# Kernel optimization log

Measured on AMD Instinct MI355X. Metric: run time of the kernel, lower is better.

Reference implementation:

```python
import jax, jax.numpy as jnp
from jax import lax
import numpy as np

B, CIN, COUT, N, H, W = 16, 64, 64, 8, 128, 128


def setup_inputs() -> dict:
    key = jax.random.key(0)
    ks = jax.random.split(key, 6)
    s = 0.05
    return {
        "x": jax.random.normal(ks[0], (B, CIN, H, W), dtype=jnp.float32),
        "condition": jax.random.normal(ks[1], (B, CIN), dtype=jnp.float32),
        "filt_w": jax.random.normal(ks[2], (N, COUT, CIN, 3, 3), dtype=jnp.float32) * s,
        "filt_b": jax.random.normal(ks[3], (N, COUT), dtype=jnp.float32) * s,
        "sel_w": jax.random.normal(ks[4], (N, CIN), dtype=jnp.float32) * s,
        "sel_b": jax.random.normal(ks[5], (N,), dtype=jnp.float32) * s,
    }


def reference(x, condition, filt_w, filt_b, sel_w, sel_b):
    b = x.shape[0]
    # condition selector: Linear(in_channels -> num_conditions) + softmax
    logits = condition.reshape(b, -1) @ sel_w.T + sel_b          # [B, N]
    weights = jax.nn.softmax(logits, axis=-1)                    # [B, N]

    n, cout, cin, kh, kw = filt_w.shape
    # Run all N branch convs in ONE conv by stacking filters on the output-channel axis.
    kern = filt_w.reshape(n * cout, cin, kh, kw)
    y = lax.conv_general_dilated(
        x, kern, window_strides=(1, 1), padding="SAME",
        dimension_numbers=("NCHW", "OIHW", "NCHW"))              # [B, N*COUT, H, W]
    h, w = y.shape[-2], y.shape[-1]
    y = y.reshape(b, n, cout, h, w) + filt_b.reshape(1, n, cout, 1, 1)
    # softmax-gated sum over the N branches
    out = jnp.einsum("bn,bnohw->bohw", weights, y)
    return out
```

## Files before the change

kernel.cpp:

```cpp
#include <hip/hip_runtime.h>
#include <stdint.h>

#define BATCH 16
#define CIN   64
#define COUT  64
#define NBR   8
#define HH    128
#define WW    128
#define XBH   130
#define XBW   130

typedef __attribute__((ext_vector_type(8)))  short short8;
typedef __attribute__((ext_vector_type(16))) float f32x16;

__device__ __forceinline__ unsigned int f2bf_hi(float f) {
    union { float f; uint32_t u; } v; v.f = f;
    return (v.u + 0x8000u) >> 16;
}
__device__ __forceinline__ unsigned short f2bf(float f) {
    union { float f; uint32_t u; } v; v.f = f;
    uint32_t u = v.u;
    return (unsigned short)((u + 0x7FFFu + ((u >> 16) & 1u)) >> 16);
}
__device__ __forceinline__ short8 gld_frag(const unsigned short* p) {
    union { uint4 u; short8 s; } t;
    t.u = *(const uint4*)p;
    return t.s;
}
__device__ __forceinline__ short8 lds_frag(const unsigned short* p) {
    union { uint2 u[2]; short8 s; } t;
    t.u[0] = *(const uint2*)p;
    t.u[1] = *(const uint2*)(p + 4);
    return t.s;
}

__global__ __launch_bounds__(256)
void k_prep(const float* __restrict__ cond,
            const float* __restrict__ sel_w,
            const float* __restrict__ sel_b,
            const float* __restrict__ filt_w,
            const float* __restrict__ filt_b,
            unsigned short* __restrict__ wfilt,
            float* __restrict__ cbias) {
    __shared__ float4 lw4[NBR * 144];
    __shared__ float lg[NBR];
    float* lw = (float*)lw4;

    const int blk = blockIdx.x;
    const int b = blk >> 6, o = blk & 63;
    const int tid = threadIdx.x;

    const float4* src4 = (const float4*)filt_w;
    #pragma unroll
    for (int i = tid; i < NBR * 144; i += 256)
        lw4[i] = src4[((i / 144) * COUT + o) * 144 + (i % 144)];

    {
        const int lane = tid & 63, w = tid >> 6;
        const float c0 = cond[b * CIN + lane];
        #pragma unroll
        for (int k = 0; k < 2; ++k) {
            const int n = w + k * 4;
            float p = c0 * sel_w[n * CIN + lane];
            #pragma unroll
            for (int off = 32; off > 0; off >>= 1)
                p += __shfl_down(p, off, 64);
            if (lane == 0) lg[n] = p + sel_b[n];
        }
    }
    __syncthreads();

    float w8[NBR];
    {
        float m = -1e30f;
        #pragma unroll
        for (int n = 0; n < NBR; ++n) m = fmaxf(m, lg[n]);
        float s = 0.f;
        #pragma unroll
        for (int n = 0; n < NBR; ++n) { w8[n] = __expf(lg[n] - m); s += w8[n]; }
        const float inv = 1.f / s;
        #pragma unroll
        for (int n = 0; n < NBR; ++n) w8[n] *= inv;
    }

    #pragma unroll
    for (int idx = tid; idx < 576; idx += 256) {
        const int t = idx >> 6, c = idx & 63;
        float acc = 0.f;
        #pragma unroll
        for (int n = 0; n < NBR; ++n)
            acc += w8[n] * lw[n * 576 + c * 9 + t];
        wfilt[(((long)(b * 9 + t) * COUT + o) << 6) + c] = f2bf(acc);
    }
    if (tid == 0) {
        float ab = 0.f;
        #pragma unroll
        for (int n = 0; n < NBR; ++n) ab += w8[n] * filt_b[n * COUT + o];
        cbias[b * COUT + o] = ab;
    }
}

__global__ __launch_bounds__(256)
void k_cast(const float* __restrict__ x, unsigned short* __restrict__ xb) {
    const int b   = blockIdx.y;
    const int hp  = blockIdx.x;
    const int tid = threadIdx.x;
    unsigned short* dst = xb + ((long)(b * XBH + hp) * XBW) * 64;
    const bool zrow = (hp == 0) || (hp == XBH - 1);
    const int h = hp - 1;
    const long cs = (long)HH * WW;

    for (int t = tid; t < XBW * 8; t += 256) {
        const int wp = t >> 3, q = t & 7;
        uint4 v; v.x = v.y = v.z = v.w = 0u;
        if (!zrow && wp != 0 && wp != XBW - 1) {
            const float* px = x + (((long)(b * CIN + q * 8)) * HH + h) * WW + (wp - 1);
            v.x = f2bf_hi(px[0])      | (f2bf_hi(px[cs])     << 16);
            v.y = f2bf_hi(px[2 * cs]) | (f2bf_hi(px[3 * cs]) << 16);
            v.z = f2bf_hi(px[4 * cs]) | (f2bf_hi(px[5 * cs]) << 16);
            v.w = f2bf_hi(px[6 * cs]) | (f2bf_hi(px[7 * cs]) << 16);
        }
        *(uint4*)&dst[t * 8] = v;
    }
}

#define RT 8
#define WT 32
#define SLABW 34
#define SLABR 10
#define PSTR  68

__global__ __launch_bounds__(256, 2)
void k_conv4(const unsigned short* __restrict__ xb,
             const unsigned short* __restrict__ wfilt,
             const float* __restrict__ cbias,
             float* __restrict__ out) {
    __shared__ unsigned short lx[SLABR * SLABW * PSTR];

    const int b  = blockIdx.z;
    const int h0 = blockIdx.y * RT;
    const int w0 = blockIdx.x * WT;
    const int tid = threadIdx.x;

    const unsigned short* xbb = xb + (long)b * XBH * XBW * 64;
    for (int t = tid; t < SLABR * SLABW * 8; t += 256) {
        const int s = t / (SLABW * 8);
        const int i = t - s * (SLABW * 8);
        const int p = i >> 3;
        const int q = i & 7;
        const uint4 v = *(const uint4*)(xbb + (((h0 + s) * XBW + w0 + p) << 6) + (q << 3));
        uint2 u0, u1;
        u0.x = v.x; u0.y = v.y; u1.x = v.z; u1.y = v.w;
        unsigned short* lp = &lx[(s * SLABW + p) * PSTR + (q << 3)];
        *(uint2*)lp       = u0;
        *(uint2*)(lp + 4) = u1;
    }

    const int lane = tid & 63;
    const int wave = tid >> 6;
    const int l31  = lane & 31;
    const int lh   = lane >> 5;
    const int r0   = wave * 2;

    const unsigned short* wf = wfilt + (long)b * 9 * COUT * CIN;

    short8 A0[4], A1[4];
    #pragma unroll
    for (int cc = 0; cc < 4; ++cc) {
        A0[cc] = gld_frag(wf + l31 * CIN + cc * 16 + lh * 8);
        A1[cc] = gld_frag(wf + (32 + l31) * CIN + cc * 16 + lh * 8);
    }

    f32x16 acc00, acc01, acc10, acc11;
    #pragma unroll
    for (int i = 0; i < 16; ++i) {
        const int m = (i & 3) + 8 * (i >> 2) + 4 * lh;
        const float b0 = cbias[b * COUT + m];
        const float b1 = cbias[b * COUT + 32 + m];
        acc00[i] = b0; acc01[i] = b0;
        acc10[i] = b1; acc11[i] = b1;
    }

    __syncthreads();

    #pragma unroll
    for (int tap = 0; tap < 9; ++tap) {
        short8 nA0[4], nA1[4];
        if (tap < 8) {
            const unsigned short* wn = wf + (long)(tap + 1) * COUT * CIN;
            #pragma unroll
            for (int cc = 0; cc < 4; ++cc) {
                nA0[cc] = gld_frag(wn + l31 * CIN + cc * 16 + lh * 8);
                nA1[cc] = gld_frag(wn + (32 + l31) * CIN + cc * 16 + lh * 8);
            }
        }
        const int kh = tap / 3, kw = tap % 3;
        #pragma unroll
        for (int cc = 0; cc < 4; ++cc) {
            const int kofs = cc * 16 + lh * 8;
            short8 b0 = lds_frag(&lx[((r0     + kh) * SLABW + l31 + kw) * PSTR + kofs]);
            short8 b1 = lds_frag(&lx[((r0 + 1 + kh) * SLABW + l31 + kw) * PSTR + kofs]);
            acc00 = __builtin_amdgcn_mfma_f32_32x32x16_bf16(A0[cc], b0, acc00, 0, 0, 0);
            acc01 = __builtin_amdgcn_mfma_f32_32x32x16_bf16(A0[cc], b1, acc01, 0, 0, 0);
            acc10 = __builtin_amdgcn_mfma_f32_32x32x16_bf16(A1[cc], b0, acc10, 0, 0, 0);
            acc11 = __builtin_amdgcn_mfma_f32_32x32x16_bf16(A1[cc], b1, acc11, 0, 0, 0);
        }
        #pragma unroll
        for (int cc = 0; cc < 4; ++cc) { A0[cc] = nA0[cc]; A1[cc] = nA1[cc]; }
    }

    #pragma unroll
    for (int cb = 0; cb < 2; ++cb) {
        #pragma unroll
        for (int pb = 0; pb < 2; ++pb) {
            const f32x16 v = cb == 0 ? (pb == 0 ? acc00 : acc01)
                                     : (pb == 0 ? acc10 : acc11);
            const int hrow = h0 + r0 + pb;
            float* op = out + (((long)(b * COUT + cb * 32) * HH + hrow) * WW + w0 + l31);
            #pragma unroll
            for (int i = 0; i < 16; ++i) {
                const int m = (i & 3) + 8 * (i >> 2) + 4 * lh;
                op[(long)m * HH * WW] = v[i];
            }
        }
    }
}

extern "C" void kernel_launch(void* const* d_in, const int* in_sizes, int n_in,
                              void* d_out, int out_size, void* d_ws, size_t ws_size,
                              hipStream_t stream) {
    const float* x      = (const float*)d_in[0];
    const float* cond   = (const float*)d_in[1];
    const float* filt_w = (const float*)d_in[2];
    const float* filt_b = (const float*)d_in[3];
    const float* sel_w  = (const float*)d_in[4];
    const float* sel_b  = (const float*)d_in[5];
    float* out = (float*)d_out;

    float*          cbias = (float*)d_ws;
    unsigned short* wfilt = (unsigned short*)((char*)d_ws + 4096);
    unsigned short* xb    = (unsigned short*)((char*)d_ws + 4096 + 1179648);

    k_prep<<<BATCH * COUT, 256, 0, stream>>>(cond, sel_w, sel_b, filt_w, filt_b, wfilt, cbias);

    dim3 cg(XBH, BATCH);
    k_cast<<<cg, 256, 0, stream>>>(x, xb);

    dim3 grid(WW / WT, HH / RT, BATCH);
    k_conv4<<<grid, 256, 0, stream>>>(xb, wfilt, cbias, out);
}
```

Measured before the change: 184.1 us.

## Pre-tile input slabs with swizzle, load via global_load_lds, merge prep kernels

The prep and cast kernels are merged into one launch. The cast half now writes the bf16 input pre-arranged as per-tile halo slabs with an XOR swizzle on the channel groups. The conv kernel copies each slab straight into LDS using global_load_lds 16-byte transfers and reads B fragments as single 128-bit LDS loads, with the swizzle intended to avoid bank conflicts. Occupancy hint rises to 3 blocks per SM because the unpadded LDS footprint is smaller. In exchange, the halo duplication makes the intermediate buffer larger and the cast does more global writes.

```diff
diff --git a/kernel.cpp b/kernel.cpp
--- a/kernel.cpp
+++ b/kernel.cpp
@@ -7,8 +7,14 @@
 #define NBR   8
 #define HH    128
 #define WW    128
-#define XBH   130
-#define XBW   130
+
+#define RT 8
+#define WT 32
+#define SLABW 34
+#define SLABR 10
+#define SLABPIX (SLABR * SLABW)
+#define SLABUS  (SLABPIX * 64)
+#define NTILES  (BATCH * (HH / RT) * (WW / WT))
 
 typedef __attribute__((ext_vector_type(8)))  short short8;
 typedef __attribute__((ext_vector_type(16))) float f32x16;
@@ -27,133 +33,133 @@
     t.u = *(const uint4*)p;
     return t.s;
 }
-__device__ __forceinline__ short8 lds_frag(const unsigned short* p) {
-    union { uint2 u[2]; short8 s; } t;
-    t.u[0] = *(const uint2*)p;
-    t.u[1] = *(const uint2*)(p + 4);
+__device__ __forceinline__ short8 lds_frag128(const unsigned short* p) {
+    union { uint4 u; short8 s; } t;
+    t.u = *(const uint4*)p;
     return t.s;
 }
+__device__ __forceinline__ void gload_lds16(const unsigned short* g, unsigned short* l) {
+    __builtin_amdgcn_global_load_lds(
+        (const __attribute__((address_space(1))) unsigned int*)g,
+        (__attribute__((address_space(3))) unsigned int*)l, 16, 0, 0);
+}
 
 __global__ __launch_bounds__(256)
-void k_prep(const float* __restrict__ cond,
-            const float* __restrict__ sel_w,
-            const float* __restrict__ sel_b,
-            const float* __restrict__ filt_w,
-            const float* __restrict__ filt_b,
-            unsigned short* __restrict__ wfilt,
-            float* __restrict__ cbias) {
+void k_pc(const float* __restrict__ cond,
+          const float* __restrict__ sel_w,
+          const float* __restrict__ sel_b,
+          const float* __restrict__ filt_w,
+          const float* __restrict__ filt_b,
+          const float* __restrict__ x,
+          unsigned short* __restrict__ wfilt,
+          float* __restrict__ cbias,
+          unsigned short* __restrict__ xt) {
     __shared__ float4 lw4[NBR * 144];
     __shared__ float lg[NBR];
-    float* lw = (float*)lw4;
-
-    const int blk = blockIdx.x;
-    const int b = blk >> 6, o = blk & 63;
     const int tid = threadIdx.x;
 
-    const float4* src4 = (const float4*)filt_w;
-    #pragma unroll
-    for (int i = tid; i < NBR * 144; i += 256)
-        lw4[i] = src4[((i / 144) * COUT + o) * 144 + (i % 144)];
-
-    {
-        const int lane = tid & 63, w = tid >> 6;
-        const float c0 = cond[b * CIN + lane];
-        #pragma unroll
-        for (int k = 0; k < 2; ++k) {
-            const int n = w + k * 4;
-            float p = c0 * sel_w[n * CIN + lane];
-            #pragma unroll
-            for (int off = 32; off > 0; off >>= 1)
-                p += __shfl_down(p, off, 64);
-            if (lane == 0) lg[n] = p + sel_b[n];
-        }
-    }
-    __syncthreads();
-
-    float w8[NBR];
-    {
-        float m = -1e30f;
-        #pragma unroll
-        for (int n = 0; n < NBR; ++n) m = fmaxf(m, lg[n]);
-        float s = 0.f;
-        #pragma unroll
-        for (int n = 0; n < NBR; ++n) { w8[n] = __expf(lg[n] - m); s += w8[n]; }
-        const float inv = 1.f / s;
-        #pragma unroll
-        for (int n = 0; n < NBR; ++n) w8[n] *= inv;
-    }
-
-    #pragma unroll
-    for (int idx = tid; idx < 576; idx += 256) {
-        const int t = idx >> 6, c = idx & 63;
-        float acc = 0.f;
-        #pragma unroll
-        for (int n = 0; n < NBR; ++n)
-            acc += w8[n] * lw[n * 576 + c * 9 + t];
-        wfilt[(((long)(b * 9 + t) * COUT + o) << 6) + c] = f2bf(acc);
-    }
-    if (tid == 0) {
-        float ab = 0.f;
-        #pragma unroll
-        for (int n = 0; n < NBR; ++n) ab += w8[n] * filt_b[n * COUT + o];
-        cbias[b * COUT + o] = ab;
-    }
-}
-
-__global__ __launch_bounds__(256)
-void k_cast(const float* __restrict__ x, unsigned short* __restrict__ xb) {
-    const int b   = blockIdx.y;
-    const int hp  = blockIdx.x;
+    if (blockIdx.x < NTILES) {
+        float* lw = (float*)lw4;
+        const int blk = blockIdx.x;
+        const int b = blk >> 6, o = blk & 63;
+
+        const float4* src4 = (const float4*)filt_w;
+        #pragma unroll
+        for (int i = tid; i < NBR * 144; i += 256)
+            lw4[i] = src4[((i / 144) * COUT + o) * 144 + (i % 144)];
+
+        {
+            const int lane = tid & 63, w = tid >> 6;
+            const float c0 = cond[b * CIN + lane];
+            #pragma unroll
+            for (int k = 0; k < 2; ++k) {
+                const int n = w + k * 4;
+                float p = c0 * sel_w[n * CIN + lane];
+                #pragma unroll
+                for (int off = 32; off > 0; off >>= 1)
+                    p += __shfl_down(p, off, 64);
+                if (lane == 0) lg[n] = p + sel_b[n];
+            }
+        }
+        __syncthreads();
+
+        float w8[NBR];
+        {
+            float m = -1e30f;
+            #pragma unroll
+            for (int n = 0; n < NBR; ++n) m = fmaxf(m, lg[n]);
+            float s = 0.f;
+            #pragma unroll
+            for (int n = 0; n < NBR; ++n) { w8[n] = __expf(lg[n] - m); s += w8[n]; }
+            const float inv = 1.f / s;
+            #pragma unroll
+            for (int n = 0; n < NBR; ++n) w8[n] *= inv;
+        }
+
+        #pragma unroll
+        for (int idx = tid; idx < 576; idx += 256) {
+            const int t = idx >> 6, c = idx & 63;
+            float acc = 0.f;
+            #pragma unroll
+            for (int n = 0; n < NBR; ++n)
+                acc += w8[n] * lw[n * 576 + c * 9 + t];
+            wfilt[(((long)(b * 9 + t) * COUT + o) << 6) + c] = f2bf(acc);
+        }
+        if (tid == 0) {
+            float ab = 0.f;
+            #pragma unroll
+            for (int n = 0; n < NBR; ++n) ab += w8[n] * filt_b[n * COUT + o];
+            cbias[b * COUT + o] = ab;
+        }
+    } else {
+        const int id = blockIdx.x - NTILES;
+        const int tx = id & 3, ty = (id >> 2) & 15, b = id >> 6;
+        const int h0 = ty * RT, w0 = tx * WT;
+        unsigned short* dst = xt + (long)id * SLABUS;
+        const long cs = (long)HH * WW;
+
+        for (int t = tid; t < SLABPIX * 8; t += 256) {
+            const int pix = t >> 3, q = t & 7;
+            const int s = pix / SLABW;
+            const int p = pix - s * SLABW;
+            const int h = h0 + s - 1, w = w0 + p - 1;
+            uint4 v; v.x = v.y = v.z = v.w = 0u;
+            if (h >= 0 && h < HH && w >= 0 && w < WW) {
+                const float* px = x + (((long)(b * CIN + q * 8)) * HH + h) * WW + w;
+                v.x = f2bf_hi(px[0])      | (f2bf_hi(px[cs])     << 16);
+                v.y = f2bf_hi(px[2 * cs]) | (f2bf_hi(px[3 * cs]) << 16);
+                v.z = f2bf_hi(px[4 * cs]) | (f2bf_hi(px[5 * cs]) << 16);
+                v.w = f2bf_hi(px[6 * cs]) | (f2bf_hi(px[7 * cs]) << 16);
+            }
+            *(uint4*)&dst[(size_t)(pix * 8 + (q ^ (pix & 7))) * 8] = v;
+        }
+    }
+}
+
+__global__ __launch_bounds__(256, 3)
+void k_conv(const unsigned short* __restrict__ xt,
+            const unsigned short* __restrict__ wfilt,
+            const float* __restrict__ cbias,
+            float* __restrict__ out) {
+    __shared__ uint4 lx4[SLABPIX * 8];
+    unsigned short* lx = (unsigned short*)lx4;
+
+    const int b  = blockIdx.z;
+    const int ty = blockIdx.y, tx = blockIdx.x;
+    const int h0 = ty * RT;
+    const int w0 = tx * WT;
     const int tid = threadIdx.x;
-    unsigned short* dst = xb + ((long)(b * XBH + hp) * XBW) * 64;
-    const bool zrow = (hp == 0) || (hp == XBH - 1);
-    const int h = hp - 1;
-    const long cs = (long)HH * WW;
-
-    for (int t = tid; t < XBW * 8; t += 256) {
-        const int wp = t >> 3, q = t & 7;
-        uint4 v; v.x = v.y = v.z = v.w = 0u;
-        if (!zrow && wp != 0 && wp != XBW - 1) {
-            const float* px = x + (((long)(b * CIN + q * 8)) * HH + h) * WW + (wp - 1);
-            v.x = f2bf_hi(px[0])      | (f2bf_hi(px[cs])     << 16);
-            v.y = f2bf_hi(px[2 * cs]) | (f2bf_hi(px[3 * cs]) << 16);
-            v.z = f2bf_hi(px[4 * cs]) | (f2bf_hi(px[5 * cs]) << 16);
-            v.w = f2bf_hi(px[6 * cs]) | (f2bf_hi(px[7 * cs]) << 16);
-        }
-        *(uint4*)&dst[t * 8] = v;
-    }
-}
-
-#define RT 8
-#define WT 32
-#define SLABW 34
-#define SLABR 10
-#define PSTR  68
-
-__global__ __launch_bounds__(256, 2)
-void k_conv4(const unsigned short* __restrict__ xb,
-             const unsigned short* __restrict__ wfilt,
-             const float* __restrict__ cbias,
-             float* __restrict__ out) {
-    __shared__ unsigned short lx[SLABR * SLABW * PSTR];
-
-    const int b  = blockIdx.z;
-    const int h0 = blockIdx.y * RT;
-    const int w0 = blockIdx.x * WT;
-    const int tid = threadIdx.x;
-
-    const unsigned short* xbb = xb + (long)b * XBH * XBW * 64;
-    for (int t = tid; t < SLABR * SLABW * 8; t += 256) {
-        const int s = t / (SLABW * 8);
-        const int i = t - s * (SLABW * 8);
-        const int p = i >> 3;
-        const int q = i & 7;
-        const uint4 v = *(const uint4*)(xbb + (((h0 + s) * XBW + w0 + p) << 6) + (q << 3));
-        uint2 u0, u1;
-        u0.x = v.x; u0.y = v.y; u1.x = v.z; u1.y = v.w;
-        unsigned short* lp = &lx[(s * SLABW + p) * PSTR + (q << 3)];
-        *(uint2*)lp       = u0;
-        *(uint2*)(lp + 4) = u1;
+    const int tile = (b * 16 + ty) * 4 + tx;
+    const unsigned short* src = xt + (long)tile * SLABUS;
+
+    #pragma unroll
+    for (int k = 0; k < 10; ++k) {
+        const int t = tid + k * 256;
+        gload_lds16(src + (size_t)t * 8, lx + (size_t)t * 8);
+    }
+    if (tid < SLABPIX * 8 - 2560) {
+        const int t = tid + 2560;
+        gload_lds16(src + (size_t)t * 8, lx + (size_t)t * 8);
     }
 
     const int lane = tid & 63;
@@ -195,11 +201,13 @@
             }
         }
         const int kh = tap / 3, kw = tap % 3;
+        const int pix0 = (r0 + kh) * SLABW + l31 + kw;
+        const int pix1 = pix0 + SLABW;
         #pragma unroll
         for (int cc = 0; cc < 4; ++cc) {
-            const int kofs = cc * 16 + lh * 8;
-            short8 b0 = lds_frag(&lx[((r0     + kh) * SLABW + l31 + kw) * PSTR + kofs]);
-            short8 b1 = lds_frag(&lx[((r0 + 1 + kh) * SLABW + l31 + kw) * PSTR + kofs]);
+            const int q = cc * 2 + lh;
+            short8 b0 = lds_frag128(lx + (size_t)pix0 * 64 + ((q ^ (pix0 & 7)) << 3));
+            short8 b1 = lds_frag128(lx + (size_t)pix1 * 64 + ((q ^ (pix1 & 7)) << 3));
             acc00 = __builtin_amdgcn_mfma_f32_32x32x16_bf16(A0[cc], b0, acc00, 0, 0, 0);
             acc01 = __builtin_amdgcn_mfma_f32_32x32x16_bf16(A0[cc], b1, acc01, 0, 0, 0);
             acc10 = __builtin_amdgcn_mfma_f32_32x32x16_bf16(A1[cc], b0, acc10, 0, 0, 0);
@@ -239,13 +247,11 @@
 
     float*          cbias = (float*)d_ws;
     unsigned short* wfilt = (unsigned short*)((char*)d_ws + 4096);
-    unsigned short* xb    = (unsigned short*)((char*)d_ws + 4096 + 1179648);
-
-    k_prep<<<BATCH * COUT, 256, 0, stream>>>(cond, sel_w, sel_b, filt_w, filt_b, wfilt, cbias);
-
-    dim3 cg(XBH, BATCH);
-    k_cast<<<cg, 256, 0, stream>>>(x, xb);
+    unsigned short* xt    = (unsigned short*)((char*)d_ws + 4096 + 1179648);
+
+    k_pc<<<NTILES * 2, 256, 0, stream>>>(cond, sel_w, sel_b, filt_w, filt_b, x,
+                                         wfilt, cbias, xt);
 
     dim3 grid(WW / WT, HH / RT, BATCH);
-    k_conv4<<<grid, 256, 0, stream>>>(xb, wfilt, cbias, out);
-}
+    k_conv<<<grid, 256, 0, stream>>>(xt, wfilt, cbias, out);
+}
```

Result: slower. 205.5 us (+11.6%).

## Merge prep and cast kernels, pad xb layout, use direct global-to-LDS loads

Applied to the files above, without the earlier changes.

Fuses the weight-prep and input-cast kernels into a single launch by splitting the block index range between the two jobs, which removes one kernel launch. The cast now writes the padded bf16 input with a 68-element pixel stride, matching the conv kernel's LDS layout. This lets the conv kernel stage its slab with contiguous 16-byte global_load_lds transfers instead of loading through registers and then storing to LDS. Occupancy is raised to 3 blocks per CU. In exchange the intermediate buffer grows by about 6%.

```diff
diff --git a/kernel.cpp b/kernel.cpp
--- a/kernel.cpp
+++ b/kernel.cpp
@@ -9,6 +9,8 @@
 #define WW    128
 #define XBH   130
 #define XBW   130
+#define PSTR  68
+#define NTILES 1024
 
 typedef __attribute__((ext_vector_type(8)))  short short8;
 typedef __attribute__((ext_vector_type(16))) float f32x16;
@@ -33,94 +35,108 @@
     t.u[1] = *(const uint2*)(p + 4);
     return t.s;
 }
+__device__ __forceinline__ void gload_lds16(const unsigned short* g, unsigned short* l) {
+    __builtin_amdgcn_global_load_lds(
+        (const __attribute__((address_space(1))) unsigned int*)g,
+        (__attribute__((address_space(3))) unsigned int*)l, 16, 0, 0);
+}
 
 __global__ __launch_bounds__(256)
-void k_prep(const float* __restrict__ cond,
-            const float* __restrict__ sel_w,
-            const float* __restrict__ sel_b,
-            const float* __restrict__ filt_w,
-            const float* __restrict__ filt_b,
-            unsigned short* __restrict__ wfilt,
-            float* __restrict__ cbias) {
+void k_pc(const float* __restrict__ cond,
+          const float* __restrict__ sel_w,
+          const float* __restrict__ sel_b,
+          const float* __restrict__ filt_w,
+          const float* __restrict__ filt_b,
+          const float* __restrict__ x,
+          unsigned short* __restrict__ wfilt,
+          float* __restrict__ cbias,
+          unsigned short* __restrict__ xb) {
     __shared__ float4 lw4[NBR * 144];
     __shared__ float lg[NBR];
-    float* lw = (float*)lw4;
-
-    const int blk = blockIdx.x;
-    const int b = blk >> 6, o = blk & 63;
     const int tid = threadIdx.x;
 
-    const float4* src4 = (const float4*)filt_w;
-    #pragma unroll
-    for (int i = tid; i < NBR * 144; i += 256)
-        lw4[i] = src4[((i / 144) * COUT + o) * 144 + (i % 144)];
-
-    {
-        const int lane = tid & 63, w = tid >> 6;
-        const float c0 = cond[b * CIN + lane];
-        #pragma unroll
-        for (int k = 0; k < 2; ++k) {
-            const int n = w + k * 4;
-            float p = c0 * sel_w[n * CIN + lane];
-            #pragma unroll
-            for (int off = 32; off > 0; off >>= 1)
-                p += __shfl_down(p, off, 64);
-            if (lane == 0) lg[n] = p + sel_b[n];
-        }
-    }
-    __syncthreads();
-
-    float w8[NBR];
-    {
-        float m = -1e30f;
-        #pragma unroll
-        for (int n = 0; n < NBR; ++n) m = fmaxf(m, lg[n]);
-        float s = 0.f;
-        #pragma unroll
-        for (int n = 0; n < NBR; ++n) { w8[n] = __expf(lg[n] - m); s += w8[n]; }
-        const float inv = 1.f / s;
-        #pragma unroll
-        for (int n = 0; n < NBR; ++n) w8[n] *= inv;
-    }
-
-    #pragma unroll
-    for (int idx = tid; idx < 576; idx += 256) {
-        const int t = idx >> 6, c = idx & 63;
-        float acc = 0.f;
-        #pragma unroll
-        for (int n = 0; n < NBR; ++n)
-            acc += w8[n] * lw[n * 576 + c * 9 + t];
-        wfilt[(((long)(b * 9 + t) * COUT + o) << 6) + c] = f2bf(acc);
-    }
-    if (tid == 0) {
-        float ab = 0.f;
-        #pragma unroll
-        for (int n = 0; n < NBR; ++n) ab += w8[n] * filt_b[n * COUT + o];
-        cbias[b * COUT + o] = ab;
-    }
-}
-
-__global__ __launch_bounds__(256)
-void k_cast(const float* __restrict__ x, unsigned short* __restrict__ xb) {
-    const int b   = blockIdx.y;
-    const int hp  = blockIdx.x;
-    const int tid = threadIdx.x;
-    unsigned short* dst = xb + ((long)(b * XBH + hp) * XBW) * 64;
-    const bool zrow = (hp == 0) || (hp == XBH - 1);
-    const int h = hp - 1;
-    const long cs = (long)HH * WW;
-
-    for (int t = tid; t < XBW * 8; t += 256) {
-        const int wp = t >> 3, q = t & 7;
-        uint4 v; v.x = v.y = v.z = v.w = 0u;
-        if (!zrow && wp != 0 && wp != XBW - 1) {
-            const float* px = x + (((long)(b * CIN + q * 8)) * HH + h) * WW + (wp - 1);
-            v.x = f2bf_hi(px[0])      | (f2bf_hi(px[cs])     << 16);
-            v.y = f2bf_hi(px[2 * cs]) | (f2bf_hi(px[3 * cs]) << 16);
-            v.z = f2bf_hi(px[4 * cs]) | (f2bf_hi(px[5 * cs]) << 16);
-            v.w = f2bf_hi(px[6 * cs]) | (f2bf_hi(px[7 * cs]) << 16);
-        }
-        *(uint4*)&dst[t * 8] = v;
+    if (blockIdx.x < NTILES) {
+        float* lw = (float*)lw4;
+        const int blk = blockIdx.x;
+        const int b = blk >> 6, o = blk & 63;
+
+        const float4* src4 = (const float4*)filt_w;
+        #pragma unroll
+        for (int i = tid; i < NBR * 144; i += 256)
+            lw4[i] = src4[((i / 144) * COUT + o) * 144 + (i % 144)];
+
+        {
+            const int lane = tid & 63, w = tid >> 6;
+            const float c0 = cond[b * CIN + lane];
+            #pragma unroll
+            for (int k = 0; k < 2; ++k) {
+                const int n = w + k * 4;
+                float p = c0 * sel_w[n * CIN + lane];
+                #pragma unroll
+                for (int off = 32; off > 0; off >>= 1)
+                    p += __shfl_down(p, off, 64);
+                if (lane == 0) lg[n] = p + sel_b[n];
+            }
+        }
+        __syncthreads();
+
+        float w8[NBR];
+        {
+            float m = -1e30f;
+            #pragma unroll
+            for (int n = 0; n < NBR; ++n) m = fmaxf(m, lg[n]);
+            float s = 0.f;
+            #pragma unroll
+            for (int n = 0; n < NBR; ++n) { w8[n] = __expf(lg[n] - m); s += w8[n]; }
+            const float inv = 1.f / s;
+            #pragma unroll
+            for (int n = 0; n < NBR; ++n) w8[n] *= inv;
+        }
+
+        #pragma unroll
+        for (int idx = tid; idx < 576; idx += 256) {
+            const int t = idx >> 6, c = idx & 63;
+            float acc = 0.f;
+            #pragma unroll
+            for (int n = 0; n < NBR; ++n)
+                acc += w8[n] * lw[n * 576 + c * 9 + t];
+            wfilt[(((long)(b * 9 + t) * COUT + o) << 6) + c] = f2bf(acc);
+        }
+        if (tid == 0) {
+            float ab = 0.f;
+            #pragma unroll
+            for (int n = 0; n < NBR; ++n) ab += w8[n] * filt_b[n * COUT + o];
+            cbias[b * COUT + o] = ab;
+        }
+    } else {
+        const int id = blockIdx.x - NTILES;
+        const int hp = id % XBH;
+        const int b  = id / XBH;
+        unsigned short* dst = xb + (long)(b * XBH + hp) * XBW * PSTR;
+        const bool zrow = (hp == 0) || (hp == XBH - 1);
+        const int h = hp - 1;
+        const long cs = (long)HH * WW;
+
+        for (int t = tid; t < XBW * 8; t += 256) {
+            const int wp = t >> 3, q = t & 7;
+            uint4 v; v.x = v.y = v.z = v.w = 0u;
+            if (!zrow && wp != 0 && wp != XBW - 1) {
+                const float* px = x + (((long)(b * CIN + q * 8)) * HH + h) * WW + (wp - 1);
+                v.x = f2bf_hi(px[0])      | (f2bf_hi(px[cs])     << 16);
+                v.y = f2bf_hi(px[2 * cs]) | (f2bf_hi(px[3 * cs]) << 16);
+                v.z = f2bf_hi(px[4 * cs]) | (f2bf_hi(px[5 * cs]) << 16);
+                v.w = f2bf_hi(px[6 * cs]) | (f2bf_hi(px[7 * cs]) << 16);
+            }
+            unsigned short* dp = dst + wp * PSTR + q * 8;
+            uint2 u0, u1;
+            u0.x = v.x; u0.y = v.y; u1.x = v.z; u1.y = v.w;
+            *(uint2*)dp       = u0;
+            *(uint2*)(dp + 4) = u1;
+            if (q == 7) {
+                uint2 z; z.x = z.y = 0u;
+                *(uint2*)(dst + wp * PSTR + 64) = z;
+            }
+        }
     }
 }
 
@@ -128,32 +144,30 @@
 #define WT 32
 #define SLABW 34
 #define SLABR 10
-#define PSTR  68
-
-__global__ __launch_bounds__(256, 2)
-void k_conv4(const unsigned short* __restrict__ xb,
-             const unsigned short* __restrict__ wfilt,
-             const float* __restrict__ cbias,
-             float* __restrict__ out) {
-    __shared__ unsigned short lx[SLABR * SLABW * PSTR];
+#define ROWUS (SLABW * PSTR)
+#define NCHUNK (SLABR * ROWUS / 8)
+
+__global__ __launch_bounds__(256, 3)
+void k_conv(const unsigned short* __restrict__ xb,
+            const unsigned short* __restrict__ wfilt,
+            const float* __restrict__ cbias,
+            float* __restrict__ out) {
+    __shared__ unsigned short lx[SLABR * ROWUS];
 
     const int b  = blockIdx.z;
     const int h0 = blockIdx.y * RT;
     const int w0 = blockIdx.x * WT;
     const int tid = threadIdx.x;
 
-    const unsigned short* xbb = xb + (long)b * XBH * XBW * 64;
-    for (int t = tid; t < SLABR * SLABW * 8; t += 256) {
-        const int s = t / (SLABW * 8);
-        const int i = t - s * (SLABW * 8);
-        const int p = i >> 3;
-        const int q = i & 7;
-        const uint4 v = *(const uint4*)(xbb + (((h0 + s) * XBW + w0 + p) << 6) + (q << 3));
-        uint2 u0, u1;
-        u0.x = v.x; u0.y = v.y; u1.x = v.z; u1.y = v.w;
-        unsigned short* lp = &lx[(s * SLABW + p) * PSTR + (q << 3)];
-        *(uint2*)lp       = u0;
-        *(uint2*)(lp + 4) = u1;
+    const unsigned short* srcb = xb + ((long)(b * XBH + h0) * XBW + w0) * PSTR;
+    #pragma unroll
+    for (int k = 0; k < 12; ++k) {
+        const int t = tid + k * 256;
+        if (t < NCHUNK) {
+            const int row = t / 289;
+            const int rc  = t - row * 289;
+            gload_lds16(srcb + (long)row * (XBW * PSTR) + rc * 8, lx + t * 8);
+        }
     }
 
     const int lane = tid & 63;
@@ -241,11 +255,9 @@
     unsigned short* wfilt = (unsigned short*)((char*)d_ws + 4096);
     unsigned short* xb    = (unsigned short*)((char*)d_ws + 4096 + 1179648);
 
-    k_prep<<<BATCH * COUT, 256, 0, stream>>>(cond, sel_w, sel_b, filt_w, filt_b, wfilt, cbias);
-
-    dim3 cg(XBH, BATCH);
-    k_cast<<<cg, 256, 0, stream>>>(x, xb);
+    k_pc<<<NTILES + BATCH * XBH, 256, 0, stream>>>(cond, sel_w, sel_b, filt_w, filt_b, x,
+                                                   wfilt, cbias, xb);
 
     dim3 grid(WW / WT, HH / RT, BATCH);
-    k_conv4<<<grid, 256, 0, stream>>>(xb, wfilt, cbias, out);
-}
+    k_conv<<<grid, 256, 0, stream>>>(xb, wfilt, cbias, out);
+}
```

After: 181.2 us. About the same (-1.6%).
